# Optimization experiments

Measured on AMD Instinct MI355X. Metric: run time of the kernel, lower is better.

The kernel has to match this reference:

```python
import jax, jax.numpy as jnp
import numpy as np

N = 50000      # nodes per graph (= num hyperedges, forced by the stack ops)
E = 800000     # incidence pairs per graph
L = 16         # max nodes per hyperedge (padded with index 0)
F_IN = 128     # in_channels
D1 = 256       # dim_1
D2 = D1 // 4   # conv2 out dim = FusionAttention in_size
H_ATT = 128    # FusionAttention hidden_size
EPS = 1e-15


def setup_inputs() -> dict:
    key = jax.random.key(0)
    ks = jax.random.split(key, 32)
    inp = {}
    for i in range(4):
        inp[f"x{i}"] = jax.random.normal(ks[i], (N, F_IN), jnp.float32)
        nidx = jax.random.randint(ks[4 + i], (E,), 0, N, dtype=jnp.int32)
        eidx = jax.random.randint(ks[8 + i], (E,), 0, N, dtype=jnp.int32)
        inp[f"ei{i}"] = jnp.stack([nidx, eidx])  # [2, E]
        hn = jax.random.randint(ks[12 + i], (N, L), 0, N + 1, dtype=jnp.int32)
        inp[f"hnode{i}"] = hn
        # hye_len = number of real (non-padding) entries per hyperedge
        inp[f"hlen{i}"] = jnp.sum(hn > 0, axis=1, keepdims=True).astype(jnp.float32)
    # shared Hgnn params (PyG HypergraphConv: lin without bias + separate bias)
    inp["W1"] = jax.random.normal(ks[16], (F_IN, D1), jnp.float32) / np.sqrt(F_IN).astype(np.float32)
    inp["b1"] = jnp.zeros((D1,), jnp.float32)
    inp["W2"] = jax.random.normal(ks[17], (D1, D2), jnp.float32) / np.sqrt(D1).astype(np.float32)
    inp["b2"] = jnp.zeros((D2,), jnp.float32)
    # two FusionAttention heads: Linear(D2,H_ATT)+Tanh, Linear(H_ATT,1,bias=False)
    for name, a, b in [("ac", 18, 19), ("am", 20, 21)]:
        inp[f"{name}_W1"] = jax.random.normal(ks[a], (D2, H_ATT), jnp.float32) / np.sqrt(D2).astype(np.float32)
        inp[f"{name}_b1"] = jnp.zeros((H_ATT,), jnp.float32)
        inp[f"{name}_W2"] = jax.random.normal(ks[b], (H_ATT, 1), jnp.float32) / np.sqrt(H_ATT).astype(np.float32)
    return inp


def _hconv(x, node_idx, edge_idx, W, b):
    """PyG HypergraphConv (heads=1, unit hyperedge weights):
    X' = D^-1 H B^-1 H^T (X W) + b, via two segment-sum passes."""
    x = x @ W  # [N, out]
    ones = jnp.ones(node_idx.shape, x.dtype)
    deg_n = jax.ops.segment_sum(ones, node_idx, num_segments=N)
    d_inv = jnp.where(deg_n > 0, 1.0 / deg_n, 0.0)
    deg_e = jax.ops.segment_sum(ones, edge_idx, num_segments=N)
    b_inv = jnp.where(deg_e > 0, 1.0 / deg_e, 0.0)
    # node -> hyperedge: m_e = B^-1[e] * sum_{v in e} x[v]
    efeat = b_inv[:, None] * jax.ops.segment_sum(x[node_idx], edge_idx, num_segments=N)
    # hyperedge -> node: out_v = D^-1[v] * sum_{e : v in e} m_e
    out = d_inv[:, None] * jax.ops.segment_sum(efeat[edge_idx], node_idx, num_segments=N)
    return out + b


def _hgnn(x, ei, W1, b1, W2, b2):
    x = jax.nn.relu(_hconv(x, ei[0], ei[1], W1, b1))
    return jax.nn.relu(_hconv(x, ei[0], ei[1], W2, b2))


def _hye_emb(node_emb, hlen, hnode):
    # prepend zero row so padding index 0 gathers zeros
    padded = jnp.concatenate([jnp.zeros((1, node_emb.shape[1]), node_emb.dtype), node_emb], axis=0)
    seq = padded[hnode]                    # [M, L, F]
    return jnp.sum(seq, axis=1) / (hlen + EPS)


def _fusion_attn(z, W1, b1, W2):
    # z: [N, 4, d]
    w = (jnp.tanh(z @ W1 + b1) @ W2).mean(0)      # [4, 1]
    beta = jax.nn.softmax(w, axis=0)              # [4, 1]
    return jnp.sum(beta * z, axis=1)              # [N, d]


def reference(x0, x1, x2, x3, ei0, ei1, ei2, ei3,
              hlen0, hlen1, hlen2, hlen3, hnode0, hnode1, hnode2, hnode3,
              W1, b1, W2, b2, ac_W1, ac_b1, ac_W2, am_W1, am_b1, am_W2):
    x1_cm = _hgnn(x0, ei0, W1, b1, W2, b2)
    x1_mc = _hgnn(x1, ei1, W1, b1, W2, b2)
    x1_cc = _hgnn(x2, ei2, W1, b1, W2, b2)
    x1_mm = _hgnn(x3, ei3, W1, b1, W2, b2)
    x2_cm = _hye_emb(x1_cm, hlen0, hnode0)
    x2_mc = _hye_emb(x1_mc, hlen1, hnode1)
    x2_cc = _hye_emb(x1_cc, hlen2, hnode2)
    x2_mm = _hye_emb(x1_mm, hlen3, hnode3)
    x_c = jnp.stack((x1_mc, x2_cm, x1_cc, x2_cc), axis=1)  # [N, 4, D2]
    x_m = jnp.stack((x1_cm, x2_mc, x1_mm, x2_mm), axis=1)
    h_c = _fusion_attn(x_c, ac_W1, ac_b1, ac_W2)
    h_m = _fusion_attn(x_m, am_W1, am_b1, am_W2)
    return (h_c, h_m)
```

## Files before the change

kernel.cpp:

```cpp
#include <hip/hip_runtime.h>
#include <hip/hip_bf16.h>

#define NF   128
#define DD1  256
#define DD2  64
#define HATT 128

static inline int cdiv(int a, int b) { return (a + b - 1) / b; }

__global__ __launch_bounds__(256) void count_rank(const int* __restrict__ nidx,
                                                  const int* __restrict__ eidx,
                                                  int* __restrict__ deg,
                                                  int* __restrict__ rank,
                                                  int N, int E) {
    int e = blockIdx.x * 256 + threadIdx.x;
    if (e < E) {
        const int vn = nidx[e], ve = eidx[e];
        const int rn = atomicAdd(&deg[vn], 1);
        const int re = atomicAdd(&deg[N + ve], 1);
        rank[e] = rn | (re << 16);
    }
}

__global__ __launch_bounds__(256) void scan_blocks(const int* __restrict__ in,
                                                   int* __restrict__ out,
                                                   int* __restrict__ partials, int n) {
    __shared__ int s[256];
    const int base = blockIdx.x * 1024;
    const int t = threadIdx.x;
    int v[4], sum = 0;
#pragma unroll
    for (int i = 0; i < 4; i++) {
        const int idx = base + t * 4 + i;
        v[i] = (idx < n) ? in[idx] : 0;
        sum += v[i];
    }
    s[t] = sum;
    __syncthreads();
    for (int o = 1; o < 256; o <<= 1) {
        int x = 0;
        if (t >= o) x = s[t - o];
        __syncthreads();
        if (t >= o) s[t] += x;
        __syncthreads();
    }
    if (t == 255) partials[blockIdx.x] = s[255];
    int run = (t == 0) ? 0 : s[t - 1];
#pragma unroll
    for (int i = 0; i < 4; i++) {
        const int idx = base + t * 4 + i;
        if (idx < n) out[idx] = run;
        run += v[i];
    }
}

__global__ __launch_bounds__(512) void scan_partials(int* __restrict__ partials, int P) {
    __shared__ int s[512];
    const int t = threadIdx.x;
    s[t] = (t < P) ? partials[t] : 0;
    __syncthreads();
    for (int o = 1; o < 512; o <<= 1) {
        int x = 0;
        if (t >= o) x = s[t - o];
        __syncthreads();
        if (t >= o) s[t] += x;
        __syncthreads();
    }
    if (t < P) partials[t] = (t == 0) ? 0 : s[t - 1];
}

__global__ __launch_bounds__(256) void scan_add(int* __restrict__ off,
                                                const int* __restrict__ partials,
                                                int n, int total) {
    const int idx = blockIdx.x * 256 + threadIdx.x;
    if (idx < n) off[idx] += partials[idx >> 10];
    if (idx == 0) off[n] = total;
}

__global__ __launch_bounds__(256) void build_fill(const int* __restrict__ nidx,
                                                  const int* __restrict__ eidx,
                                                  const int* __restrict__ rank,
                                                  const int* __restrict__ off,
                                                  int* __restrict__ srcidx,
                                                  int N, int E, int shardSize) {
    const int shard = blockIdx.x & 7;
    const int chunk = blockIdx.x >> 3;
    const int lo = shard * shardSize;
    const int hi = lo + shardSize;
    const int base = chunk * 1024;
#pragma unroll
    for (int i = 0; i < 4; i++) {
        const int e = base + i * 256 + threadIdx.x;
        if (e < E) {
            const int vn = nidx[e], ve = eidx[e];
            const int rk = rank[e];
            if (vn >= lo && vn < hi)
                srcidx[off[vn] + (rk & 0xffff)] = ve;
            if (ve >= lo && ve < hi)
                srcidx[off[N + ve] + (rk >> 16)] = vn;
        }
    }
}

__global__ __launch_bounds__(256) void invert_deg_int(const int* __restrict__ deg,
                                                      float* __restrict__ inv, int n) {
    int t = blockIdx.x * 256 + threadIdx.x;
    if (t < n) {
        const int v = deg[t];
        inv[t] = (v > 0) ? 1.0f / (float)v : 0.f;
    }
}

struct BuildB {
    const int* nidx[4];
    const int* eidx[4];
    int* deg;
    int* rank;
    const int* off;
    int* srcidx;
    int Nn, E, shardSize;
};

__global__ __launch_bounds__(256) void count_rank_b(BuildB a) {
    const int g = blockIdx.y;
    const int e = blockIdx.x * 256 + threadIdx.x;
    if (e < a.E) {
        const int vn = a.nidx[g][e], ve = a.eidx[g][e];
        int* dg = a.deg + (size_t)g * 2 * a.Nn;
        const int rn = atomicAdd(&dg[vn], 1);
        const int re = atomicAdd(&dg[a.Nn + ve], 1);
        a.rank[(size_t)g * a.E + e] = rn | (re << 16);
    }
}

__global__ __launch_bounds__(256) void build_fill_b(BuildB a) {
    const int g = blockIdx.y;
    const int shard = blockIdx.x & 7;
    const int chunk = blockIdx.x >> 3;
    const int lo = shard * a.shardSize;
    const int hi = lo + a.shardSize;
    const int base = chunk * 1024;
    const int* __restrict__ nidx = a.nidx[g];
    const int* __restrict__ eidx = a.eidx[g];
    const int* __restrict__ rank = a.rank + (size_t)g * a.E;
    const int* __restrict__ off  = a.off + (size_t)g * 2 * a.Nn;
#pragma unroll
    for (int i = 0; i < 4; i++) {
        const int e = base + i * 256 + threadIdx.x;
        if (e < a.E) {
            const int vn = nidx[e], ve = eidx[e];
            const int rk = rank[e];
            if (vn >= lo && vn < hi)
                a.srcidx[off[vn] + (rk & 0xffff)] = ve;
            if (ve >= lo && ve < hi)
                a.srcidx[off[a.Nn + ve] + (rk >> 16)] = vn;
        }
    }
}

__global__ __launch_bounds__(256) void gather_rows_128(const float* __restrict__ src,
                                                       const int* __restrict__ off,
                                                       const int* __restrict__ srcidx,
                                                       const float* __restrict__ scale,
                                                       float* __restrict__ dst, int Nn) {
    const int row = blockIdx.x * 16 + (threadIdx.x >> 4);
    if (row >= Nn) return;
    const int c = (threadIdx.x & 15) << 2;
    const int j0 = off[row], j1 = off[row + 1];
    float4 pa = make_float4(0.f, 0.f, 0.f, 0.f);
    float4 pb = make_float4(0.f, 0.f, 0.f, 0.f);
    float4 qa = make_float4(0.f, 0.f, 0.f, 0.f);
    float4 qb = make_float4(0.f, 0.f, 0.f, 0.f);
    int j = j0;
    for (; j + 3 < j1; j += 4) {
        const int s0 = srcidx[j + 0];
        const int s1 = srcidx[j + 1];
        const int s2 = srcidx[j + 2];
        const int s3 = srcidx[j + 3];
        const float4 v0a = *(const float4*)&src[(size_t)s0 * 128 + c];
        const float4 v0b = *(const float4*)&src[(size_t)s0 * 128 + c + 64];
        const float4 v1a = *(const float4*)&src[(size_t)s1 * 128 + c];
        const float4 v1b = *(const float4*)&src[(size_t)s1 * 128 + c + 64];
        const float4 v2a = *(const float4*)&src[(size_t)s2 * 128 + c];
        const float4 v2b = *(const float4*)&src[(size_t)s2 * 128 + c + 64];
        const float4 v3a = *(const float4*)&src[(size_t)s3 * 128 + c];
        const float4 v3b = *(const float4*)&src[(size_t)s3 * 128 + c + 64];
        pa.x += v0a.x + v1a.x; pa.y += v0a.y + v1a.y;
        pa.z += v0a.z + v1a.z; pa.w += v0a.w + v1a.w;
        qa.x += v2a.x + v3a.x; qa.y += v2a.y + v3a.y;
        qa.z += v2a.z + v3a.z; qa.w += v2a.w + v3a.w;
        pb.x += v0b.x + v1b.x; pb.y += v0b.y + v1b.y;
        pb.z += v0b.z + v1b.z; pb.w += v0b.w + v1b.w;
        qb.x += v2b.x + v3b.x; qb.y += v2b.y + v3b.y;
        qb.z += v2b.z + v3b.z; qb.w += v2b.w + v3b.w;
    }
    for (; j < j1; j++) {
        const int s0 = srcidx[j];
        const float4 va = *(const float4*)&src[(size_t)s0 * 128 + c];
        const float4 vb = *(const float4*)&src[(size_t)s0 * 128 + c + 64];
        pa.x += va.x; pa.y += va.y; pa.z += va.z; pa.w += va.w;
        pb.x += vb.x; pb.y += vb.y; pb.z += vb.z; pb.w += vb.w;
    }
    float4 aca = make_float4(pa.x + qa.x, pa.y + qa.y, pa.z + qa.z, pa.w + qa.w);
    float4 acb = make_float4(pb.x + qb.x, pb.y + qb.y, pb.z + qb.z, pb.w + qb.w);
    if (scale) {
        const float s = scale[row];
        aca.x *= s; aca.y *= s; aca.z *= s; aca.w *= s;
        acb.x *= s; acb.y *= s; acb.z *= s; acb.w *= s;
    }
    *(float4*)&dst[(size_t)row * 128 + c] = aca;
    *(float4*)&dst[(size_t)row * 128 + c + 64] = acb;
}

struct Gather128H {
    const float* src[2];
    float* dst;
    const int* off;
    const int* srcidx;
    const float* dinv;
    int gbase;
    int passBase;
    int Nn;
};

__global__ __launch_bounds__(256) void gather128_h(Gather128H a) {
    const int gr = blockIdx.x * 16 + (threadIdx.x >> 4);
    if (gr >= 2 * a.Nn) return;
    const int gl = gr / a.Nn;
    const int row = gr - gl * a.Nn;
    const float* __restrict__ src = a.src[gl];
    const int ob = (a.gbase + gl) * 2 * a.Nn + a.passBase + row;
    const int c = (threadIdx.x & 15) << 2;
    const int j0 = a.off[ob], j1 = a.off[ob + 1];
    float4 pa = make_float4(0.f, 0.f, 0.f, 0.f);
    float4 pb = make_float4(0.f, 0.f, 0.f, 0.f);
    float4 qa = make_float4(0.f, 0.f, 0.f, 0.f);
    float4 qb = make_float4(0.f, 0.f, 0.f, 0.f);
    int j = j0;
    for (; j + 3 < j1; j += 4) {
        const int s0 = a.srcidx[j + 0];
        const int s1 = a.srcidx[j + 1];
        const int s2 = a.srcidx[j + 2];
        const int s3 = a.srcidx[j + 3];
        const float4 v0a = *(const float4*)&src[(size_t)s0 * 128 + c];
        const float4 v0b = *(const float4*)&src[(size_t)s0 * 128 + c + 64];
        const float4 v1a = *(const float4*)&src[(size_t)s1 * 128 + c];
        const float4 v1b = *(const float4*)&src[(size_t)s1 * 128 + c + 64];
        const float4 v2a = *(const float4*)&src[(size_t)s2 * 128 + c];
        const float4 v2b = *(const float4*)&src[(size_t)s2 * 128 + c + 64];
        const float4 v3a = *(const float4*)&src[(size_t)s3 * 128 + c];
        const float4 v3b = *(const float4*)&src[(size_t)s3 * 128 + c + 64];
        pa.x += v0a.x + v1a.x; pa.y += v0a.y + v1a.y;
        pa.z += v0a.z + v1a.z; pa.w += v0a.w + v1a.w;
        qa.x += v2a.x + v3a.x; qa.y += v2a.y + v3a.y;
        qa.z += v2a.z + v3a.z; qa.w += v2a.w + v3a.w;
        pb.x += v0b.x + v1b.x; pb.y += v0b.y + v1b.y;
        pb.z += v0b.z + v1b.z; pb.w += v0b.w + v1b.w;
        qb.x += v2b.x + v3b.x; qb.y += v2b.y + v3b.y;
        qb.z += v2b.z + v3b.z; qb.w += v2b.w + v3b.w;
    }
    for (; j < j1; j++) {
        const int s0 = a.srcidx[j];
        const float4 va = *(const float4*)&src[(size_t)s0 * 128 + c];
        const float4 vb = *(const float4*)&src[(size_t)s0 * 128 + c + 64];
        pa.x += va.x; pa.y += va.y; pa.z += va.z; pa.w += va.w;
        pb.x += vb.x; pb.y += vb.y; pb.z += vb.z; pb.w += vb.w;
    }
    float4 aca = make_float4(pa.x + qa.x, pa.y + qa.y, pa.z + qa.z, pa.w + qa.w);
    float4 acb = make_float4(pb.x + qb.x, pb.y + qb.y, pb.z + qb.z, pb.w + qb.w);
    if (a.dinv) {
        const float s = a.dinv[ob];
        aca.x *= s; aca.y *= s; aca.z *= s; aca.w *= s;
        acb.x *= s; acb.y *= s; acb.z *= s; acb.w *= s;
    }
    *(float4*)&a.dst[(size_t)gr * 128 + c] = aca;
    *(float4*)&a.dst[(size_t)gr * 128 + c + 64] = acb;
}

__global__ __launch_bounds__(256) void gather_rows_64(const float* __restrict__ src,
                                                      const int* __restrict__ off,
                                                      const int* __restrict__ srcidx,
                                                      const float* __restrict__ scale,
                                                      const float* __restrict__ post_bias,
                                                      float* __restrict__ dst, int Nn) {
    const int row = blockIdx.x * 32 + (threadIdx.x >> 3);
    if (row >= Nn) return;
    const int c = (threadIdx.x & 7) << 2;
    const int j0 = off[row], j1 = off[row + 1];
    float4 pa = make_float4(0.f, 0.f, 0.f, 0.f);
    float4 pb = make_float4(0.f, 0.f, 0.f, 0.f);
    float4 qa = make_float4(0.f, 0.f, 0.f, 0.f);
    float4 qb = make_float4(0.f, 0.f, 0.f, 0.f);
    int j = j0;
    for (; j + 3 < j1; j += 4) {
        const int s0 = srcidx[j + 0];
        const int s1 = srcidx[j + 1];
        const int s2 = srcidx[j + 2];
        const int s3 = srcidx[j + 3];
        const float4 v0a = *(const float4*)&src[(size_t)s0 * 64 + c];
        const float4 v0b = *(const float4*)&src[(size_t)s0 * 64 + c + 32];
        const float4 v1a = *(const float4*)&src[(size_t)s1 * 64 + c];
        const float4 v1b = *(const float4*)&src[(size_t)s1 * 64 + c + 32];
        const float4 v2a = *(const float4*)&src[(size_t)s2 * 64 + c];
        const float4 v2b = *(const float4*)&src[(size_t)s2 * 64 + c + 32];
        const float4 v3a = *(const float4*)&src[(size_t)s3 * 64 + c];
        const float4 v3b = *(const float4*)&src[(size_t)s3 * 64 + c + 32];
        pa.x += v0a.x + v1a.x; pa.y += v0a.y + v1a.y;
        pa.z += v0a.z + v1a.z; pa.w += v0a.w + v1a.w;
        qa.x += v2a.x + v3a.x; qa.y += v2a.y + v3a.y;
        qa.z += v2a.z + v3a.z; qa.w += v2a.w + v3a.w;
        pb.x += v0b.x + v1b.x; pb.y += v0b.y + v1b.y;
        pb.z += v0b.z + v1b.z; pb.w += v0b.w + v1b.w;
        qb.x += v2b.x + v3b.x; qb.y += v2b.y + v3b.y;
        qb.z += v2b.z + v3b.z; qb.w += v2b.w + v3b.w;
    }
    for (; j < j1; j++) {
        const int s0 = srcidx[j];
        const float4 va = *(const float4*)&src[(size_t)s0 * 64 + c];
        const float4 vb = *(const float4*)&src[(size_t)s0 * 64 + c + 32];
        pa.x += va.x; pa.y += va.y; pa.z += va.z; pa.w += va.w;
        pb.x += vb.x; pb.y += vb.y; pb.z += vb.z; pb.w += vb.w;
    }
    float4 aca = make_float4(pa.x + qa.x, pa.y + qa.y, pa.z + qa.z, pa.w + qa.w);
    float4 acb = make_float4(pb.x + qb.x, pb.y + qb.y, pb.z + qb.z, pb.w + qb.w);
    if (scale) {
        const float s = scale[row];
        aca.x *= s; aca.y *= s; aca.z *= s; aca.w *= s;
        acb.x *= s; acb.y *= s; acb.z *= s; acb.w *= s;
    }
    if (post_bias) {
        aca.x = fmaxf(aca.x + post_bias[c + 0], 0.f);
        aca.y = fmaxf(aca.y + post_bias[c + 1], 0.f);
        aca.z = fmaxf(aca.z + post_bias[c + 2], 0.f);
        aca.w = fmaxf(aca.w + post_bias[c + 3], 0.f);
        acb.x = fmaxf(acb.x + post_bias[c + 32], 0.f);
        acb.y = fmaxf(acb.y + post_bias[c + 33], 0.f);
        acb.z = fmaxf(acb.z + post_bias[c + 34], 0.f);
        acb.w = fmaxf(acb.w + post_bias[c + 35], 0.f);
    }
    *(float4*)&dst[(size_t)row * 64 + c] = aca;
    *(float4*)&dst[(size_t)row * 64 + c + 32] = acb;
}

struct Gather64B {
    const float* src[4];
    float* dst;
    const int* off;
    const int* srcidx;
    const float* dinv;
    const float* post_bias;
    int passBase;
    int Nn;
};

__global__ __launch_bounds__(256) void gather64_b(Gather64B a) {
    const int gr = blockIdx.x * 32 + (threadIdx.x >> 3);
    if (gr >= 4 * a.Nn) return;
    const int g = gr / a.Nn;
    const int row = gr - g * a.Nn;
    const float* __restrict__ src = a.src[g];
    const int ob = g * 2 * a.Nn + a.passBase + row;
    const int c = (threadIdx.x & 7) << 2;
    const int j0 = a.off[ob], j1 = a.off[ob + 1];
    float4 pa = make_float4(0.f, 0.f, 0.f, 0.f);
    float4 pb = make_float4(0.f, 0.f, 0.f, 0.f);
    float4 qa = make_float4(0.f, 0.f, 0.f, 0.f);
    float4 qb = make_float4(0.f, 0.f, 0.f, 0.f);
    int j = j0;
    for (; j + 3 < j1; j += 4) {
        const int s0 = a.srcidx[j + 0];
        const int s1 = a.srcidx[j + 1];
        const int s2 = a.srcidx[j + 2];
        const int s3 = a.srcidx[j + 3];
        const float4 v0a = *(const float4*)&src[(size_t)s0 * 64 + c];
        const float4 v0b = *(const float4*)&src[(size_t)s0 * 64 + c + 32];
        const float4 v1a = *(const float4*)&src[(size_t)s1 * 64 + c];
        const float4 v1b = *(const float4*)&src[(size_t)s1 * 64 + c + 32];
        const float4 v2a = *(const float4*)&src[(size_t)s2 * 64 + c];
        const float4 v2b = *(const float4*)&src[(size_t)s2 * 64 + c + 32];
        const float4 v3a = *(const float4*)&src[(size_t)s3 * 64 + c];
        const float4 v3b = *(const float4*)&src[(size_t)s3 * 64 + c + 32];
        pa.x += v0a.x + v1a.x; pa.y += v0a.y + v1a.y;
        pa.z += v0a.z + v1a.z; pa.w += v0a.w + v1a.w;
        qa.x += v2a.x + v3a.x; qa.y += v2a.y + v3a.y;
        qa.z += v2a.z + v3a.z; qa.w += v2a.w + v3a.w;
        pb.x += v0b.x + v1b.x; pb.y += v0b.y + v1b.y;
        pb.z += v0b.z + v1b.z; pb.w += v0b.w + v1b.w;
        qb.x += v2b.x + v3b.x; qb.y += v2b.y + v3b.y;
        qb.z += v2b.z + v3b.z; qb.w += v2b.w + v3b.w;
    }
    for (; j < j1; j++) {
        const int s0 = a.srcidx[j];
        const float4 va = *(const float4*)&src[(size_t)s0 * 64 + c];
        const float4 vb = *(const float4*)&src[(size_t)s0 * 64 + c + 32];
        pa.x += va.x; pa.y += va.y; pa.z += va.z; pa.w += va.w;
        pb.x += vb.x; pb.y += vb.y; pb.z += vb.z; pb.w += vb.w;
    }
    float4 aca = make_float4(pa.x + qa.x, pa.y + qa.y, pa.z + qa.z, pa.w + qa.w);
    float4 acb = make_float4(pb.x + qb.x, pb.y + qb.y, pb.z + qb.z, pb.w + qb.w);
    if (a.dinv) {
        const float s = a.dinv[ob];
        aca.x *= s; aca.y *= s; aca.z *= s; aca.w *= s;
        acb.x *= s; acb.y *= s; acb.z *= s; acb.w *= s;
    }
    if (a.post_bias) {
        aca.x = fmaxf(aca.x + a.post_bias[c + 0], 0.f);
        aca.y = fmaxf(aca.y + a.post_bias[c + 1], 0.f);
        aca.z = fmaxf(aca.z + a.post_bias[c + 2], 0.f);
        aca.w = fmaxf(aca.w + a.post_bias[c + 3], 0.f);
        acb.x = fmaxf(acb.x + a.post_bias[c + 32], 0.f);
        acb.y = fmaxf(acb.y + a.post_bias[c + 33], 0.f);
        acb.z = fmaxf(acb.z + a.post_bias[c + 34], 0.f);
        acb.w = fmaxf(acb.w + a.post_bias[c + 35], 0.f);
    }
    *(float4*)&a.dst[(size_t)gr * 64 + c] = aca;
    *(float4*)&a.dst[(size_t)gr * 64 + c + 32] = acb;
}

__global__ __launch_bounds__(256) void gemm1_f32(const float* __restrict__ A,
                                                 const float* __restrict__ B,
                                                 float* __restrict__ C, int M,
                                                 const float* __restrict__ dinv,
                                                 const float* __restrict__ bias) {
    __shared__ float As[32][132];
    __shared__ float Bs[32][128];
    const int tid = threadIdx.x;
    const int m0 = blockIdx.y * 128;
    const int bn = blockIdx.x * 128;
    const int rq = (tid >> 4) << 2;
    const int cq = (tid & 15) << 2;

    float acc[8][8] = {{0.f}};

    for (int k0 = 0; k0 < 128; k0 += 32) {
#pragma unroll
        for (int i = 0; i < 4; i++) {
            const int f = tid + 256 * i;
            const int r = f >> 3;
            const int q = (f & 7) << 2;
            const int grow = m0 + r;
            float4 v = make_float4(0.f, 0.f, 0.f, 0.f);
            if (grow < M) v = *(const float4*)&A[(size_t)grow * 128 + k0 + q];
            As[q + 0][r] = v.x;
            As[q + 1][r] = v.y;
            As[q + 2][r] = v.z;
            As[q + 3][r] = v.w;
        }
#pragma unroll
        for (int i = 0; i < 4; i++) {
            const int f = tid + 256 * i;
            const int r = f >> 5;
            const int c4 = (f & 31) << 2;
            *(float4*)&Bs[r][c4] = *(const float4*)&B[(size_t)(k0 + r) * 256 + bn + c4];
        }
        __syncthreads();
#pragma unroll
        for (int k = 0; k < 32; k++) {
            float av[8], bv[8];
            *(float4*)&av[0] = *(const float4*)&As[k][rq];
            *(float4*)&av[4] = *(const float4*)&As[k][rq + 64];
            *(float4*)&bv[0] = *(const float4*)&Bs[k][cq];
            *(float4*)&bv[4] = *(const float4*)&Bs[k][cq + 64];
#pragma unroll
            for (int r = 0; r < 8; r++)
#pragma unroll
                for (int c = 0; c < 8; c++)
                    acc[r][c] = fmaf(av[r], bv[c], acc[r][c]);
        }
        __syncthreads();
    }
#pragma unroll
    for (int r = 0; r < 8; r++) {
        const int grow = m0 + rq + (r & 3) + ((r >> 2) << 6);
        if (grow < M) {
            const float s = dinv[grow];
            float o[8];
#pragma unroll
            for (int c = 0; c < 4; c++)
                o[c] = fmaxf(fmaf(acc[r][c], s, bias[bn + cq + c]), 0.f);
#pragma unroll
            for (int c = 4; c < 8; c++)
                o[c] = fmaxf(fmaf(acc[r][c], s, bias[bn + 64 + cq + (c - 4)]), 0.f);
            *(float4*)&C[(size_t)grow * 256 + bn + cq] = *(float4*)&o[0];
            *(float4*)&C[(size_t)grow * 256 + bn + 64 + cq] = *(float4*)&o[4];
        }
    }
}

__global__ __launch_bounds__(256) void gemm2_f32(const float* __restrict__ A,
                                                 const float* __restrict__ B,
                                                 float* __restrict__ C, int M) {
    __shared__ float As[32][132];
    __shared__ float Bs[32][64];
    const int tid = threadIdx.x;
    const int m0 = blockIdx.y * 128;
    const int tr = (tid >> 3) << 2;
    const int tc = (tid & 7) << 3;

    float acc[4][8] = {{0.f}};

    for (int k0 = 0; k0 < 256; k0 += 32) {
#pragma unroll
        for (int i = 0; i < 4; i++) {
            const int f = tid + 256 * i;
            const int r = f >> 3;
            const int q = (f & 7) << 2;
            const int grow = m0 + r;
            float4 v = make_float4(0.f, 0.f, 0.f, 0.f);
            if (grow < M) v = *(const float4*)&A[(size_t)grow * 256 + k0 + q];
            As[q + 0][r] = v.x;
            As[q + 1][r] = v.y;
            As[q + 2][r] = v.z;
            As[q + 3][r] = v.w;
        }
#pragma unroll
        for (int i = 0; i < 2; i++) {
            const int f = tid + 256 * i;
            const int r = f >> 4;
            const int c4 = (f & 15) << 2;
            *(float4*)&Bs[r][c4] = *(const float4*)&B[(size_t)(k0 + r) * 64 + c4];
        }
        __syncthreads();
#pragma unroll
        for (int k = 0; k < 32; k++) {
            float av[4], bv[8];
            *(float4*)&av[0] = *(const float4*)&As[k][tr];
            *(float4*)&bv[0] = *(const float4*)&Bs[k][tc];
            *(float4*)&bv[4] = *(const float4*)&Bs[k][tc + 4];
#pragma unroll
            for (int r = 0; r < 4; r++)
#pragma unroll
                for (int c = 0; c < 8; c++)
                    acc[r][c] = fmaf(av[r], bv[c], acc[r][c]);
        }
        __syncthreads();
    }
#pragma unroll
    for (int r = 0; r < 4; r++) {
        const int grow = m0 + tr + r;
        if (grow < M) {
            *(float4*)&C[(size_t)grow * 64 + tc] =
                make_float4(acc[r][0], acc[r][1], acc[r][2], acc[r][3]);
            *(float4*)&C[(size_t)grow * 64 + tc + 4] =
                make_float4(acc[r][4], acc[r][5], acc[r][6], acc[r][7]);
        }
    }
}

struct Gemm12B {
    const float* A;
    const float* W1;
    const float* W2;
    const float* b1;
    const float* dinv;
    float* D;
    int Nn;
};

#define TS_LD 33

__global__ __launch_bounds__(256) void gemm12_b(Gemm12B a) {
    __shared__ float smem[9472];
    float* As  = smem;
    float* Bs  = smem + 1152;
    float* Ts  = smem;
    float* W2s = smem + 8448;

    const int M4 = 4 * a.Nn;
    const int tid = threadIdx.x;
    const int m0 = blockIdx.x * 32;
    const int rq = (tid >> 5) << 2;
    const int cq = (tid & 31) << 2;

    float acc[4][8] = {{0.f}};

    for (int k0 = 0; k0 < 128; k0 += 32) {
        {
            const int r = tid >> 3;
            const int q = (tid & 7) << 2;
            const int grow = m0 + r;
            float4 v = make_float4(0.f, 0.f, 0.f, 0.f);
            if (grow < M4) v = *(const float4*)&a.A[(size_t)grow * 128 + k0 + q];
            As[(q + 0) * 36 + r] = v.x;
            As[(q + 1) * 36 + r] = v.y;
            As[(q + 2) * 36 + r] = v.z;
            As[(q + 3) * 36 + r] = v.w;
        }
#pragma unroll
        for (int i = 0; i < 8; i++) {
            const int f = tid + 256 * i;
            const int r = f >> 6;
            const int c4 = (f & 63) << 2;
            *(float4*)&Bs[r * 256 + c4] = *(const float4*)&a.W1[(size_t)(k0 + r) * 256 + c4];
        }
        __syncthreads();
#pragma unroll
        for (int k = 0; k < 32; k++) {
            float av[4], bv[8];
            *(float4*)&av[0] = *(const float4*)&As[k * 36 + rq];
            *(float4*)&bv[0] = *(const float4*)&Bs[k * 256 + cq];
            *(float4*)&bv[4] = *(const float4*)&Bs[k * 256 + cq + 128];
#pragma unroll
            for (int r = 0; r < 4; r++)
#pragma unroll
                for (int c = 0; c < 8; c++)
                    acc[r][c] = fmaf(av[r], bv[c], acc[r][c]);
        }
        __syncthreads();
    }

    {
        float b1lo[4], b1hi[4], s[4];
#pragma unroll
        for (int j = 0; j < 4; j++) {
            b1lo[j] = a.b1[cq + j];
            b1hi[j] = a.b1[cq + 128 + j];
        }
#pragma unroll
        for (int r = 0; r < 4; r++) {
            const int gr = m0 + rq + r;
            float sv = 0.f;
            if (gr < M4) {
                const int g = gr / a.Nn;
                const int lr = gr - g * a.Nn;
                sv = a.dinv[(size_t)g * 2 * a.Nn + lr];
            }
            s[r] = sv;
        }
#pragma unroll
        for (int r = 0; r < 4; r++)
#pragma unroll
            for (int j = 0; j < 4; j++) {
                Ts[(cq + j) * TS_LD + rq + r] =
                    fmaxf(fmaf(acc[r][j], s[r], b1lo[j]), 0.f);
                Ts[(cq + 128 + j) * TS_LD + rq + r] =
                    fmaxf(fmaf(acc[r][4 + j], s[r], b1hi[j]), 0.f);
            }
    }

    const int c2 = (tid & 31) << 1;
    float d0[4] = {0.f, 0.f, 0.f, 0.f};
    float d1[4] = {0.f, 0.f, 0.f, 0.f};
    for (int kk = 0; kk < 256; kk += 16) {
        __syncthreads();
        {
            const int r = tid >> 4;
            const int c4 = (tid & 15) << 2;
            *(float4*)&W2s[r * 64 + c4] = *(const float4*)&a.W2[(size_t)(kk + r) * 64 + c4];
        }
        __syncthreads();
#pragma unroll
        for (int k = 0; k < 16; k++) {
            const float* tr = &Ts[(kk + k) * TS_LD + rq];
            const float t0 = tr[0], t1 = tr[1], t2 = tr[2], t3 = tr[3];
            const float w0 = W2s[k * 64 + c2];
            const float w1 = W2s[k * 64 + c2 + 1];
            d0[0] = fmaf(t0, w0, d0[0]); d1[0] = fmaf(t0, w1, d1[0]);
            d0[1] = fmaf(t1, w0, d0[1]); d1[1] = fmaf(t1, w1, d1[1]);
            d0[2] = fmaf(t2, w0, d0[2]); d1[2] = fmaf(t2, w1, d1[2]);
            d0[3] = fmaf(t3, w0, d0[3]); d1[3] = fmaf(t3, w1, d1[3]);
        }
    }
#pragma unroll
    for (int r = 0; r < 4; r++) {
        const int gr = m0 + rq + r;
        if (gr < M4)
            *(float2*)&a.D[(size_t)gr * 64 + c2] = make_float2(d0[r], d1[r]);
    }
}

__global__ __launch_bounds__(256) void hye_emb_kernel(const float* __restrict__ emb,
                                                      const int* __restrict__ hnode,
                                                      const float* __restrict__ hlen,
                                                      float* __restrict__ out, int Nn) {
    const int r = blockIdx.x * 16 + (threadIdx.x >> 4);
    const int c = (threadIdx.x & 15) << 2;
    if (r >= Nn) return;
    const int4* hp4 = (const int4*)&hnode[(size_t)r * 16];
    const int4 w0 = hp4[0], w1 = hp4[1], w2 = hp4[2], w3 = hp4[3];
    int idx[16] = {w0.x, w0.y, w0.z, w0.w, w1.x, w1.y, w1.z, w1.w,
                   w2.x, w2.y, w2.z, w2.w, w3.x, w3.y, w3.z, w3.w};
    float4 a0 = make_float4(0.f, 0.f, 0.f, 0.f);
    float4 a1 = make_float4(0.f, 0.f, 0.f, 0.f);
    float4 a2 = make_float4(0.f, 0.f, 0.f, 0.f);
    float4 a3 = make_float4(0.f, 0.f, 0.f, 0.f);
#pragma unroll
    for (int l = 0; l < 16; l += 4) {
        if (idx[l + 0] > 0) {
            const float4 v = *(const float4*)&emb[(size_t)(idx[l + 0] - 1) * 64 + c];
            a0.x += v.x; a0.y += v.y; a0.z += v.z; a0.w += v.w;
        }
        if (idx[l + 1] > 0) {
            const float4 v = *(const float4*)&emb[(size_t)(idx[l + 1] - 1) * 64 + c];
            a1.x += v.x; a1.y += v.y; a1.z += v.z; a1.w += v.w;
        }
        if (idx[l + 2] > 0) {
            const float4 v = *(const float4*)&emb[(size_t)(idx[l + 2] - 1) * 64 + c];
            a2.x += v.x; a2.y += v.y; a2.z += v.z; a2.w += v.w;
        }
        if (idx[l + 3] > 0) {
            const float4 v = *(const float4*)&emb[(size_t)(idx[l + 3] - 1) * 64 + c];
            a3.x += v.x; a3.y += v.y; a3.z += v.z; a3.w += v.w;
        }
    }
    const float inv = 1.0f / (hlen[r] + 1e-15f);
    float4 acc;
    acc.x = (a0.x + a1.x + a2.x + a3.x) * inv;
    acc.y = (a0.y + a1.y + a2.y + a3.y) * inv;
    acc.z = (a0.z + a1.z + a2.z + a3.z) * inv;
    acc.w = (a0.w + a1.w + a2.w + a3.w) * inv;
    *(float4*)&out[(size_t)r * 64 + c] = acc;
}

struct HyeB {
    const float* emb;
    const int* hnode[4];
    const float* hlen[4];
    float* out;
    int Nn;
};

__global__ __launch_bounds__(256) void hye_b(HyeB a) {
    const int gr = blockIdx.x * 16 + (threadIdx.x >> 4);
    const int c = (threadIdx.x & 15) << 2;
    if (gr >= 4 * a.Nn) return;
    const int g = gr / a.Nn;
    const int lr = gr - g * a.Nn;
    const float* __restrict__ emb = a.emb + (size_t)g * a.Nn * 64;
    const int4* hp4 = (const int4*)&a.hnode[g][(size_t)lr * 16];
    const int4 w0 = hp4[0], w1 = hp4[1], w2 = hp4[2], w3 = hp4[3];
    int idx[16] = {w0.x, w0.y, w0.z, w0.w, w1.x, w1.y, w1.z, w1.w,
                   w2.x, w2.y, w2.z, w2.w, w3.x, w3.y, w3.z, w3.w};
    float4 a0 = make_float4(0.f, 0.f, 0.f, 0.f);
    float4 a1 = make_float4(0.f, 0.f, 0.f, 0.f);
    float4 a2 = make_float4(0.f, 0.f, 0.f, 0.f);
    float4 a3 = make_float4(0.f, 0.f, 0.f, 0.f);
#pragma unroll
    for (int l = 0; l < 16; l += 4) {
        if (idx[l + 0] > 0) {
            const float4 v = *(const float4*)&emb[(size_t)(idx[l + 0] - 1) * 64 + c];
            a0.x += v.x; a0.y += v.y; a0.z += v.z; a0.w += v.w;
        }
        if (idx[l + 1] > 0) {
            const float4 v = *(const float4*)&emb[(size_t)(idx[l + 1] - 1) * 64 + c];
            a1.x += v.x; a1.y += v.y; a1.z += v.z; a1.w += v.w;
        }
        if (idx[l + 2] > 0) {
            const float4 v = *(const float4*)&emb[(size_t)(idx[l + 2] - 1) * 64 + c];
            a2.x += v.x; a2.y += v.y; a2.z += v.z; a2.w += v.w;
        }
        if (idx[l + 3] > 0) {
            const float4 v = *(const float4*)&emb[(size_t)(idx[l + 3] - 1) * 64 + c];
            a3.x += v.x; a3.y += v.y; a3.z += v.z; a3.w += v.w;
        }
    }
    const float inv = 1.0f / (a.hlen[g][lr] + 1e-15f);
    float4 acc;
    acc.x = (a0.x + a1.x + a2.x + a3.x) * inv;
    acc.y = (a0.y + a1.y + a2.y + a3.y) * inv;
    acc.z = (a0.z + a1.z + a2.z + a3.z) * inv;
    acc.w = (a0.w + a1.w + a2.w + a3.w) * inv;
    *(float4*)&a.out[(size_t)gr * 64 + c] = acc;
}

struct AttnArgs {
    const float* z[8];
    const float* W1c; const float* b1c; const float* W2c;
    const float* W1m; const float* b1m; const float* W2m;
    float* accw;
    int Nn;
};

__global__ __launch_bounds__(256) void attn_gemm(AttnArgs a) {
    __shared__ float As[64][68];
    __shared__ float Bs[64][128];
    __shared__ float red[4];
    const int tid = threadIdx.x;
    const int gy = blockIdx.y;
    const int head = gy >> 2;
    const float* __restrict__ z  = a.z[gy];
    const float* __restrict__ W1 = head ? a.W1m : a.W1c;
    const float* __restrict__ b1 = head ? a.b1m : a.b1c;
    const float* __restrict__ W2 = head ? a.W2m : a.W2c;
    const int m0 = blockIdx.x * 64;

    {
        const int m = tid >> 2;
        const int qb = tid & 3;
        const int grow = m0 + m;
#pragma unroll
        for (int it = 0; it < 4; it++) {
            const int q = qb + 4 * it;
            float4 v = make_float4(0.f, 0.f, 0.f, 0.f);
            if (grow < a.Nn) v = *(const float4*)&z[(size_t)grow * 64 + q * 4];
            As[q * 4 + 0][m] = v.x;
            As[q * 4 + 1][m] = v.y;
            As[q * 4 + 2][m] = v.z;
            As[q * 4 + 3][m] = v.w;
        }
    }
    {
#pragma unroll
        for (int i = 0; i < 8; i++) {
            const int f = tid + 256 * i;
            const int r = f >> 5, cc = (f & 31) << 2;
            *(float4*)&Bs[r][cc] = *(const float4*)&W1[(size_t)r * 128 + cc];
        }
    }
    __syncthreads();

    const int mq = (tid & 15) << 2;
    const int cq = (tid >> 4) << 2;
    float acc[4][8] = {{0.f}};
    for (int k = 0; k < 64; k++) {
        float av[4], bv[8];
        *(float4*)&av[0] = *(const float4*)&As[k][mq];
        *(float4*)&bv[0] = *(const float4*)&Bs[k][cq];
        *(float4*)&bv[4] = *(const float4*)&Bs[k][cq + 64];
#pragma unroll
        for (int r = 0; r < 4; r++)
#pragma unroll
            for (int c = 0; c < 8; c++)
                acc[r][c] = fmaf(av[r], bv[c], acc[r][c]);
    }

    float w2v[8], b1v[8];
#pragma unroll
    for (int c = 0; c < 8; c++) {
        const int col = cq + (c & 3) + ((c >> 2) << 6);
        w2v[c] = W2[col];
        b1v[c] = b1[col];
    }
    float local = 0.f;
#pragma unroll
    for (int r = 0; r < 4; r++) {
        if (m0 + mq + r < a.Nn) {
#pragma unroll
            for (int c = 0; c < 8; c++) {
                float s = acc[r][c] + b1v[c];
                s = fminf(fmaxf(s, -15.f), 15.f);
                const float t = __expf(2.f * s);
                local += (1.f - 2.f / (t + 1.f)) * w2v[c];
            }
        }
    }
#pragma unroll
    for (int off = 32; off >= 1; off >>= 1) local += __shfl_down(local, off, 64);
    if ((tid & 63) == 0) red[tid >> 6] = local;
    __syncthreads();
    if (tid == 0) atomicAdd(&a.accw[gy], red[0] + red[1] + red[2] + red[3]);
}

__global__ void softmax_beta(const float* __restrict__ acc, float* __restrict__ beta,
                             float invN) {
    const int t = threadIdx.x;
    if (t < 2) {
        const float* a = acc + 4 * t;
        float* b = beta + 4 * t;
        float w[4], m = -1e30f;
#pragma unroll
        for (int i = 0; i < 4; i++) { w[i] = a[i] * invN; m = fmaxf(m, w[i]); }
        float s = 0.f;
#pragma unroll
        for (int i = 0; i < 4; i++) { w[i] = expf(w[i] - m); s += w[i]; }
#pragma unroll
        for (int i = 0; i < 4; i++) b[i] = w[i] / s;
    }
}

__global__ __launch_bounds__(256) void weighted_sum(const float* __restrict__ z0,
                                                    const float* __restrict__ z1,
                                                    const float* __restrict__ z2,
                                                    const float* __restrict__ z3,
                                                    const float* __restrict__ beta,
                                                    float* __restrict__ out, int Nn) {
    const int t = blockIdx.x * 256 + threadIdx.x;
    if (t >= Nn * 16) return;
    const float b0 = beta[0], b1 = beta[1], b2 = beta[2], b3 = beta[3];
    const float4 v0 = *(const float4*)&z0[(size_t)t * 4];
    const float4 v1 = *(const float4*)&z1[(size_t)t * 4];
    const float4 v2 = *(const float4*)&z2[(size_t)t * 4];
    const float4 v3 = *(const float4*)&z3[(size_t)t * 4];
    float4 o;
    o.x = b0 * v0.x + b1 * v1.x + b2 * v2.x + b3 * v3.x;
    o.y = b0 * v0.y + b1 * v1.y + b2 * v2.y + b3 * v3.y;
    o.z = b0 * v0.z + b1 * v1.z + b2 * v2.z + b3 * v3.z;
    o.w = b0 * v0.w + b1 * v1.w + b2 * v2.w + b3 * v3.w;
    *(float4*)&out[(size_t)t * 4] = o;
}

extern "C" void kernel_launch(void* const* d_in, const int* in_sizes, int n_in,
                              void* d_out, int out_size, void* d_ws, size_t ws_size,
                              hipStream_t stream) {
    const int Nn = in_sizes[0] / NF;
    const int E  = in_sizes[1] / 2;
    const int N2 = 2 * Nn;

    const float* x[4];
    const int*   ei[4];
    const int*   hnode[4];
    const float* hlen[4];
    for (int g = 0; g < 4; g++) {
        x[g]     = (const float*)d_in[4 * g + 0];
        ei[g]    = (const int*)d_in[4 * g + 1];
        hnode[g] = (const int*)d_in[4 * g + 2];
        hlen[g]  = (const float*)d_in[4 * g + 3];
    }
    const float* W1   = (const float*)d_in[16];
    const float* b1   = (const float*)d_in[17];
    const float* W2   = (const float*)d_in[18];
    const float* b2   = (const float*)d_in[19];
    const float* acW1 = (const float*)d_in[20];
    const float* acb1 = (const float*)d_in[21];
    const float* acW2 = (const float*)d_in[22];
    const float* amW1 = (const float*)d_in[23];
    const float* amb1 = (const float*)d_in[24];
    const float* amW2 = (const float*)d_in[25];

    const size_t fRA   = (size_t)4 * Nn * 64;
    const size_t fRB   = (size_t)4 * Nn * 128;
    const size_t fDinv = (size_t)4 * N2;
    const size_t fcnt  = fRA + fRB + fDinv + 16;
    const size_t icnt  = ((size_t)4 * N2 + 4) + 512 + (size_t)8 * E;
    const size_t need  = (fcnt + icnt) * sizeof(float) + 256;
    const bool raFitsInts = fRA * sizeof(float) >=
                            ((size_t)4 * N2 + (size_t)4 * E) * sizeof(int);

    if (need <= ws_size && raFitsInts) {
        float* ws = (float*)d_ws;
        size_t o = 0;
        float* RA   = ws + o; o += fRA;
        float* RB   = ws + o; o += fRB;
        float* dinv = ws + o; o += fDinv;
        float* accw = ws + o; o += 8;
        float* beta = ws + o; o += 8;
        int* iws = (int*)(ws + o);
        size_t io = 0;
        int* off      = iws + io; io += (size_t)4 * N2 + 4;
        int* partials = iws + io; io += 512;
        int* srcidx   = iws + io; io += (size_t)8 * E;
        int* deg  = (int*)RA;
        int* rank = deg + (size_t)4 * N2;

        const int n8 = 4 * N2;
        const int nScanBlocks = cdiv(n8, 1024);

        BuildB bb;
        for (int g = 0; g < 4; g++) { bb.nidx[g] = ei[g]; bb.eidx[g] = ei[g] + E; }
        bb.deg = deg; bb.rank = rank; bb.off = off; bb.srcidx = srcidx;
        bb.Nn = Nn; bb.E = E; bb.shardSize = cdiv(Nn, 8);

        hipMemsetAsync(deg, 0, (size_t)n8 * sizeof(int), stream);
        count_rank_b<<<dim3(cdiv(E, 256), 4), 256, 0, stream>>>(bb);
        scan_blocks<<<nScanBlocks, 256, 0, stream>>>(deg, off, partials, n8);
        scan_partials<<<1, 512, 0, stream>>>(partials, nScanBlocks);
        scan_add<<<cdiv(n8, 256), 256, 0, stream>>>(off, partials, n8, 2 * 4 * E);
        build_fill_b<<<dim3(8 * cdiv(E, 1024), 4), 256, 0, stream>>>(bb);
        invert_deg_int<<<cdiv(n8, 256), 256, 0, stream>>>(deg, dinv, n8);

        const int gh = cdiv(2 * Nn, 16);
        for (int h = 0; h < 2; h++) {
            const int gb = 2 * h;
            Gather128H p1;
            p1.src[0] = x[gb]; p1.src[1] = x[gb + 1];
            p1.dst = RA; p1.off = off; p1.srcidx = srcidx;
            p1.dinv = dinv; p1.gbase = gb; p1.passBase = Nn; p1.Nn = Nn;
            gather128_h<<<gh, 256, 0, stream>>>(p1);

            Gather128H p2;
            p2.src[0] = RA; p2.src[1] = RA + (size_t)Nn * 128;
            p2.dst = RB + (size_t)gb * Nn * 128;
            p2.off = off; p2.srcidx = srcidx;
            p2.dinv = nullptr; p2.gbase = gb; p2.passBase = 0; p2.Nn = Nn;
            gather128_h<<<gh, 256, 0, stream>>>(p2);
        }

        float* Dbuf = RA;
        Gemm12B gm;
        gm.A = RB; gm.W1 = W1; gm.W2 = W2; gm.b1 = b1;
        gm.dinv = dinv; gm.D = Dbuf; gm.Nn = Nn;
        gemm12_b<<<cdiv(4 * Nn, 32), 256, 0, stream>>>(gm);

        float* E1  = RB + (size_t)4 * Nn * 64;
        float* h2b = RB;
        Gather64B g3;
        for (int g = 0; g < 4; g++) g3.src[g] = Dbuf + (size_t)g * Nn * 64;
        g3.dst = E1; g3.off = off; g3.srcidx = srcidx;
        g3.dinv = dinv; g3.post_bias = nullptr; g3.passBase = Nn; g3.Nn = Nn;
        gather64_b<<<cdiv(4 * Nn, 32), 256, 0, stream>>>(g3);

        Gather64B g4;
        for (int g = 0; g < 4; g++) g4.src[g] = E1 + (size_t)g * Nn * 64;
        g4.dst = h2b; g4.off = off; g4.srcidx = srcidx;
        g4.dinv = dinv; g4.post_bias = b2; g4.passBase = 0; g4.Nn = Nn;
        gather64_b<<<cdiv(4 * Nn, 32), 256, 0, stream>>>(g4);

        float* hembb = RA;
        HyeB hb;
        hb.emb = h2b;
        for (int g = 0; g < 4; g++) { hb.hnode[g] = hnode[g]; hb.hlen[g] = hlen[g]; }
        hb.out = hembb; hb.Nn = Nn;
        hye_b<<<cdiv(4 * Nn, 16), 256, 0, stream>>>(hb);

        const size_t st = (size_t)Nn * 64;
        hipMemsetAsync(accw, 0, 8 * sizeof(float), stream);
        AttnArgs aa;
        aa.z[0] = h2b + 1 * st; aa.z[1] = hembb + 0 * st;
        aa.z[2] = h2b + 2 * st; aa.z[3] = hembb + 2 * st;
        aa.z[4] = h2b + 0 * st; aa.z[5] = hembb + 1 * st;
        aa.z[6] = h2b + 3 * st; aa.z[7] = hembb + 3 * st;
        aa.W1c = acW1; aa.b1c = acb1; aa.W2c = acW2;
        aa.W1m = amW1; aa.b1m = amb1; aa.W2m = amW2;
        aa.accw = accw; aa.Nn = Nn;
        attn_gemm<<<dim3(cdiv(Nn, 64), 8), 256, 0, stream>>>(aa);
        softmax_beta<<<1, 64, 0, stream>>>(accw, beta, 1.0f / (float)Nn);

        float* out = (float*)d_out;
        weighted_sum<<<cdiv(Nn * 16, 256), 256, 0, stream>>>(
            aa.z[0], aa.z[1], aa.z[2], aa.z[3], beta + 0, out, Nn);
        weighted_sum<<<cdiv(Nn * 16, 256), 256, 0, stream>>>(
            aa.z[4], aa.z[5], aa.z[6], aa.z[7], beta + 4, out + (size_t)Nn * DD2, Nn);
        return;
    }

    float* ws = (float*)d_ws;
    size_t o = 0;
    float* bufA = ws + o; o += (size_t)Nn * DD1;
    float* bufB = ws + o; o += (size_t)Nn * DD1;
    float* dinv = ws + o; o += N2;
    float* h2[4];
    float* hemb[4];
    for (int g = 0; g < 4; g++) { h2[g]   = ws + o; o += (size_t)Nn * DD2; }
    for (int g = 0; g < 4; g++) { hemb[g] = ws + o; o += (size_t)Nn * DD2; }
    float* accw = ws + o; o += 8;
    float* beta = ws + o; o += 8;
    int* iws = (int*)(ws + o);
    size_t io = 0;
    int* deg_i    = iws + io; io += N2;
    int* off      = iws + io; io += N2 + 1;
    int* partials = iws + io; io += 512;
    int* rank     = iws + io; io += E;
    int* srcidx   = iws + io; io += (size_t)2 * E;

    const int nScanBlocks = cdiv(N2, 1024);
    const int shardSize = cdiv(Nn, 8);

    for (int g = 0; g < 4; g++) {
        const int* nidx = ei[g];
        const int* eidx = ei[g] + E;
        const int* off_n = off;
        const int* off_e = off + Nn;
        const float* d_inv = dinv;
        const float* b_inv = dinv + Nn;

        hipMemsetAsync(deg_i, 0, (size_t)N2 * sizeof(int), stream);
        count_rank<<<cdiv(E, 256), 256, 0, stream>>>(nidx, eidx, deg_i, rank, Nn, E);
        scan_blocks<<<nScanBlocks, 256, 0, stream>>>(deg_i, off, partials, N2);
        scan_partials<<<1, 512, 0, stream>>>(partials, nScanBlocks);
        scan_add<<<cdiv(N2, 256), 256, 0, stream>>>(off, partials, N2, 2 * E);
        build_fill<<<8 * cdiv(E, 1024), 256, 0, stream>>>(nidx, eidx, rank, off,
                                                          srcidx, Nn, E, shardSize);
        invert_deg_int<<<cdiv(N2, 256), 256, 0, stream>>>(deg_i, dinv, N2);

        gather_rows_128<<<cdiv(Nn, 16), 256, 0, stream>>>(x[g], off_e, srcidx, b_inv, bufB, Nn);
        gather_rows_128<<<cdiv(Nn, 16), 256, 0, stream>>>(bufB, off_n, srcidx, nullptr, bufA, Nn);
        gemm1_f32<<<dim3(2, cdiv(Nn, 128)), 256, 0, stream>>>(bufA, W1, bufB, Nn, d_inv, b1);

        gemm2_f32<<<dim3(1, cdiv(Nn, 128)), 256, 0, stream>>>(bufB, W2, bufA, Nn);
        gather_rows_64<<<cdiv(Nn, 32), 256, 0, stream>>>(bufA, off_e, srcidx, b_inv,
                                                         nullptr, bufB, Nn);
        gather_rows_64<<<cdiv(Nn, 32), 256, 0, stream>>>(bufB, off_n, srcidx, d_inv,
                                                         b2, h2[g], Nn);

        hye_emb_kernel<<<cdiv(Nn, 16), 256, 0, stream>>>(h2[g], hnode[g], hlen[g], hemb[g], Nn);
    }

    hipMemsetAsync(accw, 0, 8 * sizeof(float), stream);
    AttnArgs aa;
    aa.z[0] = h2[1]; aa.z[1] = hemb[0]; aa.z[2] = h2[2]; aa.z[3] = hemb[2];
    aa.z[4] = h2[0]; aa.z[5] = hemb[1]; aa.z[6] = h2[3]; aa.z[7] = hemb[3];
    aa.W1c = acW1; aa.b1c = acb1; aa.W2c = acW2;
    aa.W1m = amW1; aa.b1m = amb1; aa.W2m = amW2;
    aa.accw = accw; aa.Nn = Nn;
    attn_gemm<<<dim3(cdiv(Nn, 64), 8), 256, 0, stream>>>(aa);
    softmax_beta<<<1, 64, 0, stream>>>(accw, beta, 1.0f / (float)Nn);

    float* out = (float*)d_out;
    weighted_sum<<<cdiv(Nn * 16, 256), 256, 0, stream>>>(h2[1], hemb[0], h2[2], hemb[2],
                                                         beta + 0, out, Nn);
    weighted_sum<<<cdiv(Nn * 16, 256), 256, 0, stream>>>(h2[0], hemb[1], h2[3], hemb[3],
                                                         beta + 4, out + (size_t)Nn * DD2, Nn);
}
```

Before: 1.706 ms.

## Enlarge fused GEMM tile to 64 rows and split second GEMM over k

The fused X·W1→ReLU→·W2 kernel now processes 64 rows per block with an 8x8 register tile, which halves the number of times W1 is reloaded per row. The second GEMM runs in two 32-row halves. In each half, threads compute 4x4 output tiles with float4 shared-memory reads, and the k range is split between two thread groups whose partial sums are reduced through shared memory. Costs are more registers (64 accumulators), more shared memory per block, more barriers, and half as many blocks.

```diff
diff --git a/kernel.cpp b/kernel.cpp
--- a/kernel.cpp
+++ b/kernel.cpp
@@ -557,34 +557,35 @@
     int Nn;
 };
 
-#define TS_LD 33
-
 __global__ __launch_bounds__(256) void gemm12_b(Gemm12B a) {
-    __shared__ float smem[9472];
+    __shared__ float smem[11264];
     float* As  = smem;
-    float* Bs  = smem + 1152;
+    float* Bs  = smem + 2176;
     float* Ts  = smem;
-    float* W2s = smem + 8448;
+    float* W2s = smem + 9216;
+    float* Rs  = smem;
 
     const int M4 = 4 * a.Nn;
     const int tid = threadIdx.x;
-    const int m0 = blockIdx.x * 32;
-    const int rq = (tid >> 5) << 2;
+    const int m0 = blockIdx.x * 64;
+    const int rq = (tid >> 5) << 3;
     const int cq = (tid & 31) << 2;
 
-    float acc[4][8] = {{0.f}};
+    float acc[8][8] = {{0.f}};
 
     for (int k0 = 0; k0 < 128; k0 += 32) {
-        {
-            const int r = tid >> 3;
-            const int q = (tid & 7) << 2;
+#pragma unroll
+        for (int i = 0; i < 2; i++) {
+            const int f = tid + 256 * i;
+            const int r = f >> 3;
+            const int q = (f & 7) << 2;
             const int grow = m0 + r;
             float4 v = make_float4(0.f, 0.f, 0.f, 0.f);
             if (grow < M4) v = *(const float4*)&a.A[(size_t)grow * 128 + k0 + q];
-            As[(q + 0) * 36 + r] = v.x;
-            As[(q + 1) * 36 + r] = v.y;
-            As[(q + 2) * 36 + r] = v.z;
-            As[(q + 3) * 36 + r] = v.w;
+            As[(q + 0) * 68 + r] = v.x;
+            As[(q + 1) * 68 + r] = v.y;
+            As[(q + 2) * 68 + r] = v.z;
+            As[(q + 3) * 68 + r] = v.w;
         }
 #pragma unroll
         for (int i = 0; i < 8; i++) {
@@ -596,12 +597,13 @@
         __syncthreads();
 #pragma unroll
         for (int k = 0; k < 32; k++) {
-            float av[4], bv[8];
-            *(float4*)&av[0] = *(const float4*)&As[k * 36 + rq];
+            float av[8], bv[8];
+            *(float4*)&av[0] = *(const float4*)&As[k * 68 + rq];
+            *(float4*)&av[4] = *(const float4*)&As[k * 68 + rq + 4];
             *(float4*)&bv[0] = *(const float4*)&Bs[k * 256 + cq];
             *(float4*)&bv[4] = *(const float4*)&Bs[k * 256 + cq + 128];
 #pragma unroll
-            for (int r = 0; r < 4; r++)
+            for (int r = 0; r < 8; r++)
 #pragma unroll
                 for (int c = 0; c < 8; c++)
                     acc[r][c] = fmaf(av[r], bv[c], acc[r][c]);
@@ -609,63 +611,95 @@
         __syncthreads();
     }
 
-    {
-        float b1lo[4], b1hi[4], s[4];
-#pragma unroll
-        for (int j = 0; j < 4; j++) {
-            b1lo[j] = a.b1[cq + j];
-            b1hi[j] = a.b1[cq + 128 + j];
-        }
-#pragma unroll
-        for (int r = 0; r < 4; r++) {
-            const int gr = m0 + rq + r;
-            float sv = 0.f;
-            if (gr < M4) {
-                const int g = gr / a.Nn;
-                const int lr = gr - g * a.Nn;
-                sv = a.dinv[(size_t)g * 2 * a.Nn + lr];
+    float b1lo[4], b1hi[4], sc[8];
+#pragma unroll
+    for (int j = 0; j < 4; j++) {
+        b1lo[j] = a.b1[cq + j];
+        b1hi[j] = a.b1[cq + 128 + j];
+    }
+#pragma unroll
+    for (int r = 0; r < 8; r++) {
+        const int grow = m0 + rq + r;
+        float sv = 0.f;
+        if (grow < M4) {
+            const int g = grow / a.Nn;
+            const int lr = grow - g * a.Nn;
+            sv = a.dinv[(size_t)g * 2 * a.Nn + lr];
+        }
+        sc[r] = sv;
+    }
+
+    const int col4 = (tid & 15) << 2;
+    const int row4 = ((tid >> 4) & 7) << 2;
+    const int kpar = tid >> 7;
+    const int myg  = tid >> 5;
+
+    for (int h = 0; h < 2; h++) {
+        __syncthreads();
+        if ((myg >> 2) == h) {
+            const int lmb = rq - 32 * h;
+#pragma unroll
+            for (int r = 0; r < 8; r++) {
+                const int lm = lmb + r;
+#pragma unroll
+                for (int j = 0; j < 4; j++) {
+                    Ts[(cq + j) * 36 + lm] =
+                        fmaxf(fmaf(acc[r][j], sc[r], b1lo[j]), 0.f);
+                    Ts[(cq + 128 + j) * 36 + lm] =
+                        fmaxf(fmaf(acc[r][4 + j], sc[r], b1hi[j]), 0.f);
+                }
             }
-            s[r] = sv;
-        }
-#pragma unroll
-        for (int r = 0; r < 4; r++)
-#pragma unroll
-            for (int j = 0; j < 4; j++) {
-                Ts[(cq + j) * TS_LD + rq + r] =
-                    fmaxf(fmaf(acc[r][j], s[r], b1lo[j]), 0.f);
-                Ts[(cq + 128 + j) * TS_LD + rq + r] =
-                    fmaxf(fmaf(acc[r][4 + j], s[r], b1hi[j]), 0.f);
+        }
+        float4 dr0 = make_float4(0.f, 0.f, 0.f, 0.f);
+        float4 dr1 = make_float4(0.f, 0.f, 0.f, 0.f);
+        float4 dr2 = make_float4(0.f, 0.f, 0.f, 0.f);
+        float4 dr3 = make_float4(0.f, 0.f, 0.f, 0.f);
+        for (int kk = 0; kk < 256; kk += 32) {
+            __syncthreads();
+#pragma unroll
+            for (int i = 0; i < 2; i++) {
+                const int f = tid + 256 * i;
+                const int r = f >> 4;
+                const int c4 = (f & 15) << 2;
+                *(float4*)&W2s[r * 64 + c4] = *(const float4*)&a.W2[(size_t)(kk + r) * 64 + c4];
             }
-    }
-
-    const int c2 = (tid & 31) << 1;
-    float d0[4] = {0.f, 0.f, 0.f, 0.f};
-    float d1[4] = {0.f, 0.f, 0.f, 0.f};
-    for (int kk = 0; kk < 256; kk += 16) {
-        __syncthreads();
-        {
-            const int r = tid >> 4;
-            const int c4 = (tid & 15) << 2;
-            *(float4*)&W2s[r * 64 + c4] = *(const float4*)&a.W2[(size_t)(kk + r) * 64 + c4];
-        }
-        __syncthreads();
-#pragma unroll
-        for (int k = 0; k < 16; k++) {
-            const float* tr = &Ts[(kk + k) * TS_LD + rq];
-            const float t0 = tr[0], t1 = tr[1], t2 = tr[2], t3 = tr[3];
-            const float w0 = W2s[k * 64 + c2];
-            const float w1 = W2s[k * 64 + c2 + 1];
-            d0[0] = fmaf(t0, w0, d0[0]); d1[0] = fmaf(t0, w1, d1[0]);
-            d0[1] = fmaf(t1, w0, d0[1]); d1[1] = fmaf(t1, w1, d1[1]);
-            d0[2] = fmaf(t2, w0, d0[2]); d1[2] = fmaf(t2, w1, d1[2]);
-            d0[3] = fmaf(t3, w0, d0[3]); d1[3] = fmaf(t3, w1, d1[3]);
-        }
-    }
-#pragma unroll
-    for (int r = 0; r < 4; r++) {
-        const int gr = m0 + rq + r;
-        if (gr < M4)
-            *(float2*)&a.D[(size_t)gr * 64 + c2] = make_float2(d0[r], d1[r]);
+            __syncthreads();
+#pragma unroll
+            for (int j = 0; j < 16; j++) {
+                const int k = 2 * j + kpar;
+                const float4 tv = *(const float4*)&Ts[(kk + k) * 36 + row4];
+                const float4 wv = *(const float4*)&W2s[k * 64 + col4];
+                dr0.x = fmaf(tv.x, wv.x, dr0.x); dr0.y = fmaf(tv.x, wv.y, dr0.y);
+                dr0.z = fmaf(tv.x, wv.z, dr0.z); dr0.w = fmaf(tv.x, wv.w, dr0.w);
+                dr1.x = fmaf(tv.y, wv.x, dr1.x); dr1.y = fmaf(tv.y, wv.y, dr1.y);
+                dr1.z = fmaf(tv.y, wv.z, dr1.z); dr1.w = fmaf(tv.y, wv.w, dr1.w);
+                dr2.x = fmaf(tv.z, wv.x, dr2.x); dr2.y = fmaf(tv.z, wv.y, dr2.y);
+                dr2.z = fmaf(tv.z, wv.z, dr2.z); dr2.w = fmaf(tv.z, wv.w, dr2.w);
+                dr3.x = fmaf(tv.w, wv.x, dr3.x); dr3.y = fmaf(tv.w, wv.y, dr3.y);
+                dr3.z = fmaf(tv.w, wv.z, dr3.z); dr3.w = fmaf(tv.w, wv.w, dr3.w);
+            }
+        }
+        __syncthreads();
+        if (kpar) {
+            *(float4*)&Rs[(row4 + 0) * 68 + col4] = dr0;
+            *(float4*)&Rs[(row4 + 1) * 68 + col4] = dr1;
+            *(float4*)&Rs[(row4 + 2) * 68 + col4] = dr2;
+            *(float4*)&Rs[(row4 + 3) * 68 + col4] = dr3;
+        }
+        __syncthreads();
+        if (!kpar) {
+            float4 part[4] = {dr0, dr1, dr2, dr3};
+#pragma unroll
+            for (int r = 0; r < 4; r++) {
+                const int grow = m0 + 32 * h + row4 + r;
+                if (grow < M4) {
+                    float4 o = *(float4*)&Rs[(row4 + r) * 68 + col4];
+                    o.x += part[r].x; o.y += part[r].y;
+                    o.z += part[r].z; o.w += part[r].w;
+                    *(float4*)&a.D[(size_t)grow * 64 + col4] = o;
+                }
+            }
+        }
     }
 }
 
@@ -979,7 +1013,7 @@
         Gemm12B gm;
         gm.A = RB; gm.W1 = W1; gm.W2 = W2; gm.b1 = b1;
         gm.dinv = dinv; gm.D = Dbuf; gm.Nn = Nn;
-        gemm12_b<<<cdiv(4 * Nn, 32), 256, 0, stream>>>(gm);
+        gemm12_b<<<cdiv(4 * Nn, 64), 256, 0, stream>>>(gm);
 
         float* E1  = RB + (size_t)4 * Nn * 64;
         float* h2b = RB;
```

New measurement: 1.831 ms. 1.07x slower.
